# Kernel tuning notes

Hardware: AMD Instinct MI355X
Metric: run time of the kernel (lower is better)

## Reference

```python
import jax, jax.numpy as jnp
import numpy as np

B, T, ENC, DEC, A = 64, 2048, 1024, 1024, 512


def setup_inputs() -> dict:
    key = jax.random.key(0)
    k1, k2, k3, k4, k5 = jax.random.split(key, 5)
    return {
        "h_j": jax.random.normal(k1, (B, T, ENC), dtype=jnp.float32),
        "s_t": jax.random.normal(k2, (B, DEC), dtype=jnp.float32),
        "U_w": jax.random.normal(k3, (ENC, A), dtype=jnp.float32) * (ENC ** -0.5),
        "W_w": jax.random.normal(k4, (DEC, A), dtype=jnp.float32) * (DEC ** -0.5),
        "V_w": jax.random.normal(k5, (A, 1), dtype=jnp.float32) * (A ** -0.5),
    }


def reference(h_j, s_t, U_w, W_w, V_w):
    # f1: [B, T, A] ; f2: [B, 1, A]
    f1 = jnp.einsum("bte,ea->bta", h_j, U_w)
    f2 = (s_t @ W_w)[:, None, :]
    # additive score e_t: [B, T, 1]
    e_t = jnp.tanh(f1 + f2) @ V_w
    a_t = jax.nn.softmax(e_t, axis=1)            # softmax over sequence axis
    c_t = jnp.sum(a_t * h_j, axis=1, keepdims=True)  # [B, 1, ENC]
    return (c_t, a_t)
```

## Files before the change

kernel.cpp:

```cpp
#include <hip/hip_runtime.h>
#include <hip/hip_bf16.h>
#include <stdint.h>

#define B_   64
#define T_   2048
#define ENC_ 1024
#define DEC_ 1024
#define A_   512
#define M_   (B_ * T_)

#define BM 128
#define BN 256
#define BK 64

typedef __bf16 bf16x8 __attribute__((ext_vector_type(8)));
typedef float  f32x4  __attribute__((ext_vector_type(4)));
typedef unsigned short u16;
typedef u16 u16x8 __attribute__((ext_vector_type(8)));

__device__ __forceinline__ float fast_tanh(float x) {
    float ax = fabsf(x);
    float e  = __expf(-2.0f * ax);
    float t  = (1.0f - e) / (1.0f + e);
    return copysignf(t, x);
}

__global__ __launch_bounds__(256) void k_transpose_U(
        const float* __restrict__ U, u16* __restrict__ Ut) {
    int idx = blockIdx.x * 256 + threadIdx.x;
    if (idx >= ENC_ * A_) return;
    int k = idx / A_, n = idx % A_;
    __bf16 v = (__bf16)U[idx];
    Ut[n * ENC_ + k] = *(u16*)&v;
}

__global__ __launch_bounds__(256) void k_f2(
        const float* __restrict__ s, const float* __restrict__ W,
        float* __restrict__ f2) {
    int b = blockIdx.x;
    int a0 = threadIdx.x;
    const float* srow = s + (size_t)b * DEC_;
    float acc0 = 0.f, acc1 = 0.f;
    for (int e = 0; e < DEC_; ++e) {
        float sv = srow[e];
        acc0 = fmaf(sv, W[(size_t)e * A_ + a0],       acc0);
        acc1 = fmaf(sv, W[(size_t)e * A_ + a0 + 256], acc1);
    }
    f2[(size_t)b * A_ + a0]       = acc0;
    f2[(size_t)b * A_ + a0 + 256] = acc1;
}

__global__ __launch_bounds__(512, 4) void k_gemm_e(
        const float* __restrict__ h, const u16* __restrict__ Ut,
        const float* __restrict__ f2, const float* __restrict__ V,
        float* __restrict__ e_part) {
    __shared__ u16 Alds[BM * BK];
    __shared__ u16 Blds[BN * BK];

    const int tid  = threadIdx.x;
    const int lane = tid & 63;
    const int wid  = tid >> 6;
    const int wr   = wid >> 2;
    const int wc   = wid & 3;
    const int lr   = lane & 15;
    const int g    = lane >> 4;
    const int sw   = (lr & 7) << 3;

    const int d    = blockIdx.x;
    const int xcd  = d & 7;
    const int s    = d >> 3;
    const int m    = s & 1;
    const int pair = xcd * 128 + (s >> 1);
    const int brow = pair * BM;
    const int bcol = m * BN;
    const int b    = brow / T_;

    f32x4 acc[4][4] = {};

    for (int kt = 0; kt < ENC_ / BK; ++kt) {
        const int k0 = kt * BK;

#pragma unroll
        for (int it = 0; it < 4; ++it) {
            int G  = it * 512 + tid;
            int n  = G >> 3;
            int kc = ((G & 7) ^ (n & 7)) << 3;
            const u16* src = Ut + (size_t)(bcol + n) * ENC_ + k0 + kc;
            u16* dst = &Blds[(size_t)(it * 512 + wid * 64) * 8];
            __builtin_amdgcn_global_load_lds(
                (const __attribute__((address_space(1))) void*)src,
                (__attribute__((address_space(3))) void*)dst, 16, 0, 0);
        }

#pragma unroll
        for (int it = 0; it < 2; ++it) {
            int flat = (it * 512 + tid) * 8;
            int r = flat >> 6, c = flat & 63;
            const float* srcA = h + (size_t)(brow + r) * ENC_ + k0 + c;
            f32x4 v0 = *(const f32x4*)srcA;
            f32x4 v1 = *(const f32x4*)(srcA + 4);
            u16x8 w;
#pragma unroll
            for (int j = 0; j < 4; ++j) {
                __bf16 lo = (__bf16)v0[j], hi = (__bf16)v1[j];
                w[j]     = *(u16*)&lo;
                w[j + 4] = *(u16*)&hi;
            }
            *(u16x8*)&Alds[flat ^ ((r & 7) << 3)] = w;
        }
        __syncthreads();

#pragma unroll
        for (int kk = 0; kk < 2; ++kk) {
            bf16x8 af[4], bfr[4];
#pragma unroll
            for (int mf = 0; mf < 4; ++mf)
                af[mf] = *(const bf16x8*)&Alds[
                    (((wr * 64 + mf * 16 + lr) * 64) + kk * 32 + g * 8) ^ sw];
#pragma unroll
            for (int nf = 0; nf < 4; ++nf)
                bfr[nf] = *(const bf16x8*)&Blds[
                    (((wc * 64 + nf * 16 + lr) * 64) + kk * 32 + g * 8) ^ sw];
#pragma unroll
            for (int mf = 0; mf < 4; ++mf)
#pragma unroll
                for (int nf = 0; nf < 4; ++nf)
                    acc[mf][nf] = __builtin_amdgcn_mfma_f32_16x16x32_bf16(
                        af[mf], bfr[nf], acc[mf][nf], 0, 0, 0);
        }
        __syncthreads();
    }

    float vv[4], ff[4];
#pragma unroll
    for (int nf = 0; nf < 4; ++nf) {
        int n = bcol + wc * 64 + nf * 16 + lr;
        vv[nf] = V[n];
        ff[nf] = f2[(size_t)b * A_ + n];
    }
    const int p = m * 4 + wc;
    float* ep = e_part + (size_t)p * M_ + brow + wr * 64;
#pragma unroll
    for (int mf = 0; mf < 4; ++mf) {
        float sums[4];
#pragma unroll
        for (int i = 0; i < 4; ++i) {
            float sv = 0.f;
#pragma unroll
            for (int nf = 0; nf < 4; ++nf) {
                float x = acc[mf][nf][i] + ff[nf];
                sv = fmaf(fast_tanh(x), vv[nf], sv);
            }
#pragma unroll
            for (int mm = 1; mm < 16; mm <<= 1)
                sv += __shfl_xor(sv, mm, 64);
            sums[i] = sv;
        }
        if (lr == 0) {
#pragma unroll
            for (int i = 0; i < 4; ++i)
                ep[mf * 16 + g * 4 + i] = sums[i];
        }
    }
}

__global__ __launch_bounds__(256) void k_softmax(
        const float* __restrict__ e_part, float* __restrict__ a_out) {
    const int b = blockIdx.x, tid = threadIdx.x;
    const int lane = tid & 63, w = tid >> 6;
    __shared__ float red[4], red2[4];

    float ls[8];
    float lmax = -1e30f;
#pragma unroll
    for (int i = 0; i < 8; ++i) {
        size_t mm = (size_t)b * T_ + i * 256 + tid;
        float sv = 0.f;
#pragma unroll
        for (int p = 0; p < 8; ++p) sv += e_part[(size_t)p * M_ + mm];
        ls[i] = sv;
        lmax = fmaxf(lmax, sv);
    }
#pragma unroll
    for (int mm = 1; mm < 64; mm <<= 1) lmax = fmaxf(lmax, __shfl_xor(lmax, mm, 64));
    if (lane == 0) red[w] = lmax;
    __syncthreads();
    float bmax = fmaxf(fmaxf(red[0], red[1]), fmaxf(red[2], red[3]));

    float lsum = 0.f;
#pragma unroll
    for (int i = 0; i < 8; ++i) { ls[i] = __expf(ls[i] - bmax); lsum += ls[i]; }
#pragma unroll
    for (int mm = 1; mm < 64; mm <<= 1) lsum += __shfl_xor(lsum, mm, 64);
    if (lane == 0) red2[w] = lsum;
    __syncthreads();
    float inv = 1.0f / (red2[0] + red2[1] + red2[2] + red2[3]);

#pragma unroll
    for (int i = 0; i < 8; ++i)
        a_out[(size_t)b * T_ + i * 256 + tid] = ls[i] * inv;
}

__global__ __launch_bounds__(256) void k_ctx_part(
        const float* __restrict__ h, const float* __restrict__ a,
        float* __restrict__ c_part) {
    const int b = blockIdx.x, tc = blockIdx.y, tid = threadIdx.x;
    __shared__ float alds[128];
    if (tid < 128)
        alds[tid] = a[(size_t)b * T_ + tc * 128 + tid];
    __syncthreads();

    float4 acc = {0.f, 0.f, 0.f, 0.f};
    const float* hb = h + ((size_t)b * T_ + (size_t)tc * 128) * ENC_ + tid * 4;
    for (int t = 0; t < 128; ++t) {
        float av = alds[t];
        float4 hv = *(const float4*)(hb + (size_t)t * ENC_);
        acc.x = fmaf(av, hv.x, acc.x);
        acc.y = fmaf(av, hv.y, acc.y);
        acc.z = fmaf(av, hv.z, acc.z);
        acc.w = fmaf(av, hv.w, acc.w);
    }
    *(float4*)&c_part[((size_t)(tc * 64 + b)) * ENC_ + tid * 4] = acc;
}

__global__ __launch_bounds__(256) void k_ctx_final(
        const float* __restrict__ c_part, float* __restrict__ c_out) {
    int idx = blockIdx.x * 256 + threadIdx.x;
    int off = idx * 4;
    float4 sv = {0.f, 0.f, 0.f, 0.f};
#pragma unroll
    for (int tc = 0; tc < 16; ++tc) {
        float4 v = *(const float4*)&c_part[(size_t)tc * 64 * 1024 + off];
        sv.x += v.x; sv.y += v.y; sv.z += v.z; sv.w += v.w;
    }
    *(float4*)&c_out[off] = sv;
}

extern "C" void kernel_launch(void* const* d_in, const int* in_sizes, int n_in,
                              void* d_out, int out_size, void* d_ws, size_t ws_size,
                              hipStream_t stream) {
    const float* h = (const float*)d_in[0];
    const float* s = (const float*)d_in[1];
    const float* U = (const float*)d_in[2];
    const float* W = (const float*)d_in[3];
    const float* V = (const float*)d_in[4];

    float* out   = (float*)d_out;
    float* c_out = out;
    float* a_out = out + 64 * 1024;

    char* ws = (char*)d_ws;
    u16*   Ut     = (u16*)ws;
    float* f2     = (float*)(ws + (1 << 20));
    float* e_part = (float*)(ws + (1 << 20) + (128 << 10));
    float* c_part = e_part;

    k_transpose_U<<<2048, 256, 0, stream>>>(U, Ut);
    k_f2<<<64, 256, 0, stream>>>(s, W, f2);

    k_gemm_e<<<2048, 512, 0, stream>>>(h, Ut, f2, V, e_part);

    k_softmax<<<64, 256, 0, stream>>>(e_part, a_out);

    dim3 gc(64, 16);
    k_ctx_part<<<gc, 256, 0, stream>>>(h, a_out, c_part);
    k_ctx_final<<<64, 256, 0, stream>>>(c_part, c_out);
}
```

Measured before the change: 346.1 us.

## Fuse score GEMM with online softmax and context accumulation per 64-row chunk

Replaces the 128x256 tiled score GEMM plus separate softmax and context kernels with one kernel per 64-row chunk that computes the full A=512 width, takes a chunk-local max and exp-sum, and accumulates the weighted context while that slice of h is still hot in cache. A small reduce kernel rescales and merges the per-chunk partials in flash-attention style, and a final kernel writes the normalized attention weights. This removes the second full pass over h (512 MB) from HBM. In exchange, every block now streams all of Ut (1 MB) through LDS, so total B traffic through L2 roughly doubles, and the larger LDS footprint may reduce occupancy. A workspace-size check keeps the old path as a fallback.

```diff
diff --git a/kernel.cpp b/kernel.cpp
--- a/kernel.cpp
+++ b/kernel.cpp
@@ -9,9 +9,10 @@
 #define A_   512
 #define M_   (B_ * T_)
 
-#define BM 128
-#define BN 256
-#define BK 64
+#define BK   64
+#define CH   64
+#define NCH  (M_ / CH)
+#define CPB  (T_ / CH)
 
 typedef __bf16 bf16x8 __attribute__((ext_vector_type(8)));
 typedef float  f32x4  __attribute__((ext_vector_type(4)));
@@ -50,40 +51,207 @@
     f2[(size_t)b * A_ + a0 + 256] = acc1;
 }
 
-__global__ __launch_bounds__(512, 4) void k_gemm_e(
+__global__ __launch_bounds__(512, 4) void k_gemm_fused(
+        const float* __restrict__ h, const u16* __restrict__ Ut,
+        const float* __restrict__ f2, const float* __restrict__ V,
+        float* __restrict__ e_full, float* __restrict__ mpart,
+        float* __restrict__ spart, float* __restrict__ opart) {
+    __shared__ u16 Alds[CH * BK];
+    __shared__ u16 Blds[A_ * BK];
+    __shared__ float ered[8][64];
+    __shared__ float wlds[64];
+
+    const int tid  = threadIdx.x;
+    const int lane = tid & 63;
+    const int wid  = tid >> 6;
+    const int lr   = lane & 15;
+    const int g    = lane >> 4;
+    const int sw   = (lr & 7) << 3;
+
+    const int d      = blockIdx.x;
+    const int gchunk = (d & 7) * 256 + (d >> 3);
+    const int brow   = gchunk * CH;
+    const int b      = gchunk >> 5;
+    const int chunk  = gchunk & 31;
+
+    f32x4 acc[4][4] = {};
+
+    for (int kt = 0; kt < ENC_ / BK; ++kt) {
+        const int k0 = kt * BK;
+#pragma unroll
+        for (int it = 0; it < 8; ++it) {
+            int G  = it * 512 + tid;
+            int n  = G >> 3;
+            int kc = ((G & 7) ^ (n & 7)) << 3;
+            const u16* src = Ut + (size_t)n * ENC_ + k0 + kc;
+            u16* dst = &Blds[(size_t)(it * 512 + wid * 64) * 8];
+            __builtin_amdgcn_global_load_lds(
+                (const __attribute__((address_space(1))) void*)src,
+                (__attribute__((address_space(3))) void*)dst, 16, 0, 0);
+        }
+        {
+            int r = tid >> 3, c = (tid & 7) * 8;
+            const float* srcA = h + (size_t)(brow + r) * ENC_ + k0 + c;
+            f32x4 v0 = *(const f32x4*)srcA;
+            f32x4 v1 = *(const f32x4*)(srcA + 4);
+            u16x8 w;
+#pragma unroll
+            for (int j = 0; j < 4; ++j) {
+                __bf16 lo = (__bf16)v0[j], hi = (__bf16)v1[j];
+                w[j]     = *(u16*)&lo;
+                w[j + 4] = *(u16*)&hi;
+            }
+            *(u16x8*)&Alds[(tid * 8) ^ ((r & 7) << 3)] = w;
+        }
+        __syncthreads();
+
+#pragma unroll
+        for (int kk = 0; kk < 2; ++kk) {
+            bf16x8 af[4], bfr[4];
+#pragma unroll
+            for (int mf = 0; mf < 4; ++mf)
+                af[mf] = *(const bf16x8*)&Alds[
+                    (((mf * 16 + lr) * 64) + kk * 32 + g * 8) ^ sw];
+#pragma unroll
+            for (int nf = 0; nf < 4; ++nf)
+                bfr[nf] = *(const bf16x8*)&Blds[
+                    (((wid * 64 + nf * 16 + lr) * 64) + kk * 32 + g * 8) ^ sw];
+#pragma unroll
+            for (int mf = 0; mf < 4; ++mf)
+#pragma unroll
+                for (int nf = 0; nf < 4; ++nf)
+                    acc[mf][nf] = __builtin_amdgcn_mfma_f32_16x16x32_bf16(
+                        af[mf], bfr[nf], acc[mf][nf], 0, 0, 0);
+        }
+        __syncthreads();
+    }
+
+    float vv[4], ff[4];
+#pragma unroll
+    for (int nf = 0; nf < 4; ++nf) {
+        int n = wid * 64 + nf * 16 + lr;
+        vv[nf] = V[n];
+        ff[nf] = f2[(size_t)b * A_ + n];
+    }
+#pragma unroll
+    for (int mf = 0; mf < 4; ++mf) {
+        float sums[4];
+#pragma unroll
+        for (int i = 0; i < 4; ++i) {
+            float sv = 0.f;
+#pragma unroll
+            for (int nf = 0; nf < 4; ++nf) {
+                float x = acc[mf][nf][i] + ff[nf];
+                sv = fmaf(fast_tanh(x), vv[nf], sv);
+            }
+#pragma unroll
+            for (int mm = 1; mm < 16; mm <<= 1)
+                sv += __shfl_xor(sv, mm, 64);
+            sums[i] = sv;
+        }
+        if (lr == 0) {
+#pragma unroll
+            for (int i = 0; i < 4; ++i)
+                ered[wid][mf * 16 + g * 4 + i] = sums[i];
+        }
+    }
+    __syncthreads();
+
+    if (tid < 64) {
+        float er = 0.f;
+#pragma unroll
+        for (int w = 0; w < 8; ++w) er += ered[w][tid];
+        float mb = er;
+#pragma unroll
+        for (int mm = 1; mm < 64; mm <<= 1)
+            mb = fmaxf(mb, __shfl_xor(mb, mm, 64));
+        float wr_ = __expf(er - mb);
+        float sb = wr_;
+#pragma unroll
+        for (int mm = 1; mm < 64; mm <<= 1)
+            sb += __shfl_xor(sb, mm, 64);
+        wlds[tid] = wr_;
+        e_full[(size_t)b * T_ + chunk * CH + tid] = er;
+        if (tid == 0) { mpart[gchunk] = mb; spart[gchunk] = sb; }
+    }
+    __syncthreads();
+
+    const int c2 = tid * 2;
+    float o0 = 0.f, o1 = 0.f;
+#pragma unroll 8
+    for (int r = 0; r < CH; ++r) {
+        float w = wlds[r];
+        float2 hv = *(const float2*)(h + (size_t)(brow + r) * ENC_ + c2);
+        o0 = fmaf(w, hv.x, o0);
+        o1 = fmaf(w, hv.y, o1);
+    }
+    float* op = opart + (size_t)gchunk * ENC_ + c2;
+    op[0] = o0; op[1] = o1;
+}
+
+__global__ __launch_bounds__(256) void k_ctx_reduce(
+        const float* __restrict__ mpart, const float* __restrict__ spart,
+        const float* __restrict__ opart, float* __restrict__ c_out,
+        float* __restrict__ mg_g, float* __restrict__ sg_g) {
+    const int b = blockIdx.x, tid = threadIdx.x;
+    __shared__ float esc[CPB];
+    __shared__ float mgS, sgS;
+
+    if (tid < CPB) {
+        float mr = mpart[b * CPB + tid];
+        float sr = spart[b * CPB + tid];
+        float mg = mr;
+#pragma unroll
+        for (int mm = 1; mm < 32; mm <<= 1)
+            mg = fmaxf(mg, __shfl_xor(mg, mm, 32));
+        float e = __expf(mr - mg);
+        esc[tid] = e;
+        float S = sr * e;
+#pragma unroll
+        for (int mm = 1; mm < 32; mm <<= 1)
+            S += __shfl_xor(S, mm, 32);
+        if (tid == 0) { mgS = mg; sgS = S; mg_g[b] = mg; sg_g[b] = S; }
+    }
+    __syncthreads();
+    float inv = 1.0f / sgS;
+    int c = tid * 4;
+    f32x4 av = {0.f, 0.f, 0.f, 0.f};
+    for (int r = 0; r < CPB; ++r) {
+        f32x4 ov = *(const f32x4*)&opart[((size_t)(b * CPB + r)) * ENC_ + c];
+        float e = esc[r];
+        av[0] = fmaf(e, ov[0], av[0]); av[1] = fmaf(e, ov[1], av[1]);
+        av[2] = fmaf(e, ov[2], av[2]); av[3] = fmaf(e, ov[3], av[3]);
+    }
+    av[0] *= inv; av[1] *= inv; av[2] *= inv; av[3] *= inv;
+    *(f32x4*)&c_out[(size_t)b * ENC_ + c] = av;
+}
+
+__global__ __launch_bounds__(256) void k_a_final(
+        const float* __restrict__ e_full, const float* __restrict__ mg_g,
+        const float* __restrict__ sg_g, float* __restrict__ a_out) {
+    int idx = blockIdx.x * 256 + threadIdx.x;
+    int b = idx >> 11;
+    a_out[idx] = __expf(e_full[idx] - mg_g[b]) / sg_g[b];
+}
+
+__global__ __launch_bounds__(512, 4) void k_gemm_e_fb(
         const float* __restrict__ h, const u16* __restrict__ Ut,
         const float* __restrict__ f2, const float* __restrict__ V,
         float* __restrict__ e_part) {
-    __shared__ u16 Alds[BM * BK];
-    __shared__ u16 Blds[BN * BK];
-
-    const int tid  = threadIdx.x;
-    const int lane = tid & 63;
-    const int wid  = tid >> 6;
-    const int wr   = wid >> 2;
-    const int wc   = wid & 3;
-    const int lr   = lane & 15;
-    const int g    = lane >> 4;
-    const int sw   = (lr & 7) << 3;
-
-    const int d    = blockIdx.x;
-    const int xcd  = d & 7;
-    const int s    = d >> 3;
-    const int m    = s & 1;
+    __shared__ u16 Alds[128 * BK];
+    __shared__ u16 Blds[256 * BK];
+    const int tid = threadIdx.x, lane = tid & 63, wid = tid >> 6;
+    const int wr = wid >> 2, wc = wid & 3, lr = lane & 15, g = lane >> 4;
+    const int sw = (lr & 7) << 3;
+    const int d = blockIdx.x, xcd = d & 7, s = d >> 3, m = s & 1;
     const int pair = xcd * 128 + (s >> 1);
-    const int brow = pair * BM;
-    const int bcol = m * BN;
-    const int b    = brow / T_;
-
+    const int brow = pair * 128, bcol = m * 256, b = brow / T_;
     f32x4 acc[4][4] = {};
-
     for (int kt = 0; kt < ENC_ / BK; ++kt) {
         const int k0 = kt * BK;
-
 #pragma unroll
         for (int it = 0; it < 4; ++it) {
-            int G  = it * 512 + tid;
-            int n  = G >> 3;
+            int G = it * 512 + tid, n = G >> 3;
             int kc = ((G & 7) ^ (n & 7)) << 3;
             const u16* src = Ut + (size_t)(bcol + n) * ENC_ + k0 + kc;
             u16* dst = &Blds[(size_t)(it * 512 + wid * 64) * 8];
@@ -91,36 +259,29 @@
                 (const __attribute__((address_space(1))) void*)src,
                 (__attribute__((address_space(3))) void*)dst, 16, 0, 0);
         }
-
 #pragma unroll
         for (int it = 0; it < 2; ++it) {
-            int flat = (it * 512 + tid) * 8;
-            int r = flat >> 6, c = flat & 63;
+            int flat = (it * 512 + tid) * 8, r = flat >> 6, c = flat & 63;
             const float* srcA = h + (size_t)(brow + r) * ENC_ + k0 + c;
-            f32x4 v0 = *(const f32x4*)srcA;
-            f32x4 v1 = *(const f32x4*)(srcA + 4);
+            f32x4 v0 = *(const f32x4*)srcA, v1 = *(const f32x4*)(srcA + 4);
             u16x8 w;
 #pragma unroll
             for (int j = 0; j < 4; ++j) {
                 __bf16 lo = (__bf16)v0[j], hi = (__bf16)v1[j];
-                w[j]     = *(u16*)&lo;
-                w[j + 4] = *(u16*)&hi;
+                w[j] = *(u16*)&lo; w[j + 4] = *(u16*)&hi;
             }
             *(u16x8*)&Alds[flat ^ ((r & 7) << 3)] = w;
         }
         __syncthreads();
-
 #pragma unroll
         for (int kk = 0; kk < 2; ++kk) {
             bf16x8 af[4], bfr[4];
 #pragma unroll
             for (int mf = 0; mf < 4; ++mf)
-                af[mf] = *(const bf16x8*)&Alds[
-                    (((wr * 64 + mf * 16 + lr) * 64) + kk * 32 + g * 8) ^ sw];
+                af[mf] = *(const bf16x8*)&Alds[(((wr * 64 + mf * 16 + lr) * 64) + kk * 32 + g * 8) ^ sw];
 #pragma unroll
             for (int nf = 0; nf < 4; ++nf)
-                bfr[nf] = *(const bf16x8*)&Blds[
-                    (((wc * 64 + nf * 16 + lr) * 64) + kk * 32 + g * 8) ^ sw];
+                bfr[nf] = *(const bf16x8*)&Blds[(((wc * 64 + nf * 16 + lr) * 64) + kk * 32 + g * 8) ^ sw];
 #pragma unroll
             for (int mf = 0; mf < 4; ++mf)
 #pragma unroll
@@ -130,13 +291,11 @@
         }
         __syncthreads();
     }
-
     float vv[4], ff[4];
 #pragma unroll
     for (int nf = 0; nf < 4; ++nf) {
         int n = bcol + wc * 64 + nf * 16 + lr;
-        vv[nf] = V[n];
-        ff[nf] = f2[(size_t)b * A_ + n];
+        vv[nf] = V[n]; ff[nf] = f2[(size_t)b * A_ + n];
     }
     const int p = m * 4 + wc;
     float* ep = e_part + (size_t)p * M_ + brow + wr * 64;
@@ -147,46 +306,37 @@
         for (int i = 0; i < 4; ++i) {
             float sv = 0.f;
 #pragma unroll
-            for (int nf = 0; nf < 4; ++nf) {
-                float x = acc[mf][nf][i] + ff[nf];
-                sv = fmaf(fast_tanh(x), vv[nf], sv);
-            }
-#pragma unroll
-            for (int mm = 1; mm < 16; mm <<= 1)
-                sv += __shfl_xor(sv, mm, 64);
+            for (int nf = 0; nf < 4; ++nf)
+                sv = fmaf(fast_tanh(acc[mf][nf][i] + ff[nf]), vv[nf], sv);
+#pragma unroll
+            for (int mm = 1; mm < 16; mm <<= 1) sv += __shfl_xor(sv, mm, 64);
             sums[i] = sv;
         }
-        if (lr == 0) {
-#pragma unroll
-            for (int i = 0; i < 4; ++i)
-                ep[mf * 16 + g * 4 + i] = sums[i];
-        }
-    }
-}
-
-__global__ __launch_bounds__(256) void k_softmax(
+        if (lr == 0)
+#pragma unroll
+            for (int i = 0; i < 4; ++i) ep[mf * 16 + g * 4 + i] = sums[i];
+    }
+}
+
+__global__ __launch_bounds__(256) void k_softmax_fb(
         const float* __restrict__ e_part, float* __restrict__ a_out) {
     const int b = blockIdx.x, tid = threadIdx.x;
     const int lane = tid & 63, w = tid >> 6;
     __shared__ float red[4], red2[4];
-
-    float ls[8];
-    float lmax = -1e30f;
+    float ls[8]; float lmax = -1e30f;
 #pragma unroll
     for (int i = 0; i < 8; ++i) {
         size_t mm = (size_t)b * T_ + i * 256 + tid;
         float sv = 0.f;
 #pragma unroll
         for (int p = 0; p < 8; ++p) sv += e_part[(size_t)p * M_ + mm];
-        ls[i] = sv;
-        lmax = fmaxf(lmax, sv);
+        ls[i] = sv; lmax = fmaxf(lmax, sv);
     }
 #pragma unroll
     for (int mm = 1; mm < 64; mm <<= 1) lmax = fmaxf(lmax, __shfl_xor(lmax, mm, 64));
     if (lane == 0) red[w] = lmax;
     __syncthreads();
     float bmax = fmaxf(fmaxf(red[0], red[1]), fmaxf(red[2], red[3]));
-
     float lsum = 0.f;
 #pragma unroll
     for (int i = 0; i < 8; ++i) { ls[i] = __expf(ls[i] - bmax); lsum += ls[i]; }
@@ -195,35 +345,30 @@
     if (lane == 0) red2[w] = lsum;
     __syncthreads();
     float inv = 1.0f / (red2[0] + red2[1] + red2[2] + red2[3]);
-
 #pragma unroll
     for (int i = 0; i < 8; ++i)
         a_out[(size_t)b * T_ + i * 256 + tid] = ls[i] * inv;
 }
 
-__global__ __launch_bounds__(256) void k_ctx_part(
+__global__ __launch_bounds__(256) void k_ctx_part_fb(
         const float* __restrict__ h, const float* __restrict__ a,
         float* __restrict__ c_part) {
     const int b = blockIdx.x, tc = blockIdx.y, tid = threadIdx.x;
     __shared__ float alds[128];
-    if (tid < 128)
-        alds[tid] = a[(size_t)b * T_ + tc * 128 + tid];
-    __syncthreads();
-
+    if (tid < 128) alds[tid] = a[(size_t)b * T_ + tc * 128 + tid];
+    __syncthreads();
     float4 acc = {0.f, 0.f, 0.f, 0.f};
     const float* hb = h + ((size_t)b * T_ + (size_t)tc * 128) * ENC_ + tid * 4;
     for (int t = 0; t < 128; ++t) {
         float av = alds[t];
         float4 hv = *(const float4*)(hb + (size_t)t * ENC_);
-        acc.x = fmaf(av, hv.x, acc.x);
-        acc.y = fmaf(av, hv.y, acc.y);
-        acc.z = fmaf(av, hv.z, acc.z);
-        acc.w = fmaf(av, hv.w, acc.w);
+        acc.x = fmaf(av, hv.x, acc.x); acc.y = fmaf(av, hv.y, acc.y);
+        acc.z = fmaf(av, hv.z, acc.z); acc.w = fmaf(av, hv.w, acc.w);
     }
     *(float4*)&c_part[((size_t)(tc * 64 + b)) * ENC_ + tid * 4] = acc;
 }
 
-__global__ __launch_bounds__(256) void k_ctx_final(
+__global__ __launch_bounds__(256) void k_ctx_final_fb(
         const float* __restrict__ c_part, float* __restrict__ c_out) {
     int idx = blockIdx.x * 256 + threadIdx.x;
     int off = idx * 4;
@@ -250,19 +395,33 @@
     float* a_out = out + 64 * 1024;
 
     char* ws = (char*)d_ws;
-    u16*   Ut     = (u16*)ws;
-    float* f2     = (float*)(ws + (1 << 20));
-    float* e_part = (float*)(ws + (1 << 20) + (128 << 10));
-    float* c_part = e_part;
+    u16*   Ut = (u16*)ws;
+    float* f2 = (float*)(ws + (1 << 20));
 
     k_transpose_U<<<2048, 256, 0, stream>>>(U, Ut);
     k_f2<<<64, 256, 0, stream>>>(s, W, f2);
 
-    k_gemm_e<<<2048, 512, 0, stream>>>(h, Ut, f2, V, e_part);
-
-    k_softmax<<<64, 256, 0, stream>>>(e_part, a_out);
-
-    dim3 gc(64, 16);
-    k_ctx_part<<<gc, 256, 0, stream>>>(h, a_out, c_part);
-    k_ctx_final<<<64, 256, 0, stream>>>(c_part, c_out);
-}
+    const size_t NEED = (size_t)10 * 1024 * 1024 + (64 << 10);
+    if (ws_size >= NEED) {
+        float* e_full = (float*)(ws + 0x120000);
+        float* mpart  = (float*)(ws + 0x1A0000);
+        float* spart  = (float*)(ws + 0x1A2000);
+        float* mg_g   = (float*)(ws + 0x1A4000);
+        float* sg_g   = (float*)(ws + 0x1A4100);
+        float* opart  = (float*)(ws + 0x200000);
+
+        k_gemm_fused<<<NCH, 512, 0, stream>>>(h, Ut, f2, V,
+                                              e_full, mpart, spart, opart);
+        k_ctx_reduce<<<64, 256, 0, stream>>>(mpart, spart, opart,
+                                             c_out, mg_g, sg_g);
+        k_a_final<<<M_ / 256, 256, 0, stream>>>(e_full, mg_g, sg_g, a_out);
+    } else {
+        float* e_part = (float*)(ws + (1 << 20) + (128 << 10));
+        float* c_part = e_part;
+        k_gemm_e_fb<<<2048, 512, 0, stream>>>(h, Ut, f2, V, e_part);
+        k_softmax_fb<<<64, 256, 0, stream>>>(e_part, a_out);
+        dim3 gc(64, 16);
+        k_ctx_part_fb<<<gc, 256, 0, stream>>>(h, a_out, c_part);
+        k_ctx_final_fb<<<64, 256, 0, stream>>>(c_part, c_out);
+    }
+}
```

Result: faster. 322.6 us (-6.8%).
